# Kernel tuning notes

Hardware: AMD Instinct MI355X
Metric: run time of the kernel (lower is better)

The kernel has to match this reference:

```python
import jax, jax.numpy as jnp
import numpy as np

N_NODES, N_EDGES = 10000, 100000
NODE_DIM, NUM_BASIS = 128, 20
MULS = {0: 128, 1: 64, 2: 32}            # 128x0e + 64x1e + 32x2e
NUM_IRREPS = 224                          # total multiplicity count
HIDDEN = NODE_DIM + NUM_IRREPS            # 352
SPH_DIM = 128 * 1 + 64 * 3 + 32 * 5       # 480
LN_EPS = 1e-5

def _s2_basis():
    # orthonormal (Frobenius) basis of symmetric traceless 3x3 matrices (real l=2)
    s = np.zeros((5, 3, 3)); r2 = 1.0 / np.sqrt(2.0)
    s[0, 0, 1] = s[0, 1, 0] = r2
    s[1, 1, 2] = s[1, 2, 1] = r2
    s[2] = np.diag([-1.0, -1.0, 2.0]) / np.sqrt(6.0)
    s[3, 0, 2] = s[3, 2, 0] = r2
    s[4] = np.diag([1.0, -1.0, 0.0]) * r2
    return s

def _cg_tables():
    # real Clebsch-Gordan tensors for l<=2 built from the invariant tensors
    # delta, Levi-Civita, and the symmetric-traceless basis; unit Frobenius norm (e3nn w3j convention)
    e3 = np.zeros((3, 3, 3))
    e3[0, 1, 2] = e3[1, 2, 0] = e3[2, 0, 1] = 1.0
    e3[0, 2, 1] = e3[2, 1, 0] = e3[1, 0, 2] = -1.0
    S = _s2_basis(); I3 = np.eye(3); I5 = np.eye(5)
    nrm = lambda c: (c / np.linalg.norm(c)).astype(np.float32)
    cg = {(0, 0, 0): np.ones((1, 1, 1), np.float32)}
    cg[(0, 1, 1)] = nrm(I3[None]); cg[(1, 0, 1)] = nrm(I3[:, None, :]); cg[(1, 1, 0)] = nrm(I3[:, :, None])
    cg[(0, 2, 2)] = nrm(I5[None]); cg[(2, 0, 2)] = nrm(I5[:, None, :]); cg[(2, 2, 0)] = nrm(I5[:, :, None])
    cg[(1, 1, 1)] = nrm(e3)
    cg[(1, 1, 2)] = nrm(np.transpose(S, (1, 2, 0)))
    cg[(1, 2, 1)] = nrm(np.transpose(S, (1, 0, 2)))
    cg[(2, 1, 1)] = nrm(S)
    cg[(2, 2, 1)] = nrm(np.einsum('ijk,Mil,Nlj->MNk', e3, S, S))
    cg[(1, 2, 2)] = nrm(np.einsum('iab,Mac,Ncb->iMN', e3, S, S))
    cg[(2, 1, 2)] = nrm(np.einsum('jab,Mac,Ncb->MjN', e3, S, S))
    cg[(2, 2, 2)] = nrm(np.einsum('Mab,Nbc,Pca->MNP', S, S, S))
    return cg

CG = _cg_tables()
PATHS = [(0, 0, 0), (1, 1, 0), (2, 2, 0),
         (0, 1, 1), (1, 0, 1), (1, 1, 1), (1, 2, 1), (2, 1, 1), (2, 2, 1),
         (0, 2, 2), (1, 1, 2), (1, 2, 2), (2, 0, 2), (2, 1, 2), (2, 2, 2)]
FAN = {0: 224, 1: 384, 2: 352}   # e3nn 'element' path-norm fan-in per output irrep
TP_NUMW = sum(MULS[l1] * MULS[l3] for (l1, _, l3) in PATHS)

def _layernorm(x, w, b):
    mu = x.mean(-1, keepdims=True)
    var = ((x - mu) ** 2).mean(-1, keepdims=True)
    return (x - mu) * jax.lax.rsqrt(var + LN_EPS) * w + b

def _o3_layernorm(x, w, b):
    # equivariant layer norm: per-irrep RMS over (mul, m); mean-centering + bias only for scalars
    n = x.shape[0]; outs = []; off = 0; woff = 0
    for l in (0, 1, 2):
        mul, d = MULS[l], 2 * l + 1
        f = x[:, off:off + mul * d].reshape(n, mul, d)
        if l == 0:
            f = f - f.mean(axis=1, keepdims=True)
        nrm = (f * f).mean(axis=(1, 2), keepdims=True)
        f = f * jax.lax.rsqrt(nrm + LN_EPS) * w[woff:woff + mul][None, :, None]
        if l == 0:
            f = f + b[None, :, None]
        outs.append(f.reshape(n, mul * d)); off += mul * d; woff += mul
    return jnp.concatenate(outs, -1)

def _fc_tp(x1, x2, tp_w):
    # FullyConnectedTensorProduct(128x0e+64x1e+32x2e, 1x0e+1x1e+1x2e -> 128x0e+64x1e+32x2e)
    outs = {0: 0.0, 1: 0.0, 2: 0.0}; off = 0
    for (l1, l2, l3) in PATHS:
        m1, m3 = MULS[l1], MULS[l3]
        W = tp_w[off:off + m1 * m3].reshape(m1, m3); off += m1 * m3
        pw = float(np.sqrt((2 * l3 + 1) / FAN[l3]))
        outs[l3] = outs[l3] + pw * jnp.einsum('eum,en,mnk,uw->ewk', x1[l1], x2[l2], jnp.asarray(CG[(l1, l2, l3)]), W, optimize=True)
    e = x2[0].shape[0]
    return jnp.concatenate([outs[l].reshape(e, -1) for l in (0, 1, 2)], -1)

def _forward(x_scalar, x_spherical, rbf, rsh, ln_w, ln_b, o3_w, o3_b,
             mlp_w1, mlp_b1, mlp_w2, mlp_b2, rbf_w, tp_w, edge_index):
    scalar_in = _layernorm(x_scalar, ln_w, ln_b)                # [N,128]
    spherical_in = _o3_layernorm(x_spherical, o3_w, o3_b)       # [N,480]
    h = jax.nn.silu(scalar_in @ mlp_w1 + mlp_b1)
    scalar_out = h @ mlp_w2 + mlp_b2                            # [N,352]
    filt = rbf @ rbf_w                                          # [E,352]
    dst, src = edge_index[0], edge_index[1]
    fo = scalar_out[src] * filt                                 # gather + RBF filter
    gate, msg_scalar = fo[:, :NUM_IRREPS], fo[:, NUM_IRREPS:]
    sph = spherical_in[src]                                     # [E,480]
    e = sph.shape[0]
    # ElementwiseTensorProduct(edge_irreps, 224x0e): per-channel scalar gating
    x1 = {0: (sph[:, :128] * gate[:, :128])[:, :, None],
          1: sph[:, 128:320].reshape(e, 64, 3) * gate[:, 128:192, None],
          2: sph[:, 320:480].reshape(e, 32, 5) * gate[:, 192:224, None]}
    x2 = {0: rsh[:, :1], 1: rsh[:, 1:4], 2: rsh[:, 4:9]}
    msg_sph = _fc_tp(x1, x2, tp_w)                              # [E,480]
    new_scalar = scalar_in.at[dst].add(msg_scalar)
    new_spherical = spherical_in.at[dst].add(msg_sph)
    return new_scalar, new_spherical

def setup_inputs():
    key = jax.random.key(0)
    ks = jax.random.split(key, 9)
    return {
        'x_scalar': jax.random.normal(ks[0], (N_NODES, NODE_DIM), jnp.float32),
        'x_spherical': jax.random.normal(ks[1], (N_NODES, SPH_DIM), jnp.float32),
        'rbf': jax.random.uniform(ks[2], (N_EDGES, NUM_BASIS), jnp.float32),
        'rsh': jax.random.normal(ks[3], (N_EDGES, 9), jnp.float32),
        'edge_index': jax.random.randint(ks[4], (2, N_EDGES), 0, N_NODES, dtype=jnp.int32),
        'ln_w': jnp.ones((NODE_DIM,), jnp.float32),
        'ln_b': jnp.zeros((NODE_DIM,), jnp.float32),
        'o3_w': jnp.ones((NUM_IRREPS,), jnp.float32),
        'o3_b': jnp.zeros((128,), jnp.float32),
        'mlp_w1': jax.random.normal(ks[5], (NODE_DIM, NODE_DIM), jnp.float32) / np.sqrt(NODE_DIM),
        'mlp_b1': jnp.zeros((NODE_DIM,), jnp.float32),
        'mlp_w2': jax.random.normal(ks[6], (NODE_DIM, HIDDEN), jnp.float32) / np.sqrt(NODE_DIM),
        'mlp_b2': jnp.zeros((HIDDEN,), jnp.float32),
        'rbf_w': jax.random.normal(ks[7], (NUM_BASIS, HIDDEN), jnp.float32) / np.sqrt(NUM_BASIS),
        'tp_w': jax.random.normal(ks[8], (TP_NUMW,), jnp.float32),
    }

def reference(x_scalar, x_spherical, rbf, rsh, edge_index, ln_w, ln_b, o3_w, o3_b,
              mlp_w1, mlp_b1, mlp_w2, mlp_b2, rbf_w, tp_w):
    return _forward(x_scalar, x_spherical, rbf, rsh, ln_w, ln_b, o3_w, o3_b,
                    mlp_w1, mlp_b1, mlp_w2, mlp_b2, rbf_w, tp_w, edge_index)
```

## Files before the change

kernel.cpp:

```cpp
#include <hip/hip_runtime.h>

#define NN 10000
#define NE 100000
#define ND 128
#define NB 20
#define NIR 224
#define NH 352
#define SD 480
#define BS 512
#define ET 16
#define NTILES (NE / ET)

#define CR   0.70710678118654752f
#define CA   0.40824829046386302f
#define HA   0.20412414523193151f
#define HR   0.35355339059327376f
#define C110 0.57735026918962576f
#define C220 0.44721359549995794f
#define C111 0.40824829046386302f
#define C11X 0.44721359549995794f
#define C221 0.36514837167011074f
#define C222 0.58554004376912270f
#define S32  0.86602540378443865f
#define PW0  0.066815310478106094f
#define PW1  0.088388347648318447f
#define PW2  0.11918321088232916f

typedef __bf16 v8bf __attribute__((ext_vector_type(8)));
typedef unsigned short us8v __attribute__((ext_vector_type(8)));
typedef float f32x4 __attribute__((ext_vector_type(4)));

__device__ __forceinline__ unsigned short f2bfc(float f) {
  __bf16 h = (__bf16)f;
  return __builtin_bit_cast(unsigned short, h);
}
__device__ __forceinline__ float bf2f(unsigned short h) {
  unsigned int u = ((unsigned int)h) << 16;
  return __builtin_bit_cast(float, u);
}

__device__ __forceinline__ float warpReduceSum(float v) {
  #pragma unroll
  for (int off = 32; off > 0; off >>= 1) v += __shfl_down(v, off, 64);
  return v;
}

__device__ __forceinline__ int t2tT(int t) {
  if (t < 128) return t;
  if (t < 320) { int c = t - 128; return 128 + (c % 3) * 64 + c / 3; }
  int c = t - 320; return 320 + (c % 5) * 32 + c / 5;
}

__global__ __launch_bounds__(256) void sort_hist(const int* __restrict__ ei, int* __restrict__ cnt) {
  int e = blockIdx.x * 256 + threadIdx.x;
  if (e < NE) atomicAdd(&cnt[ei[e]], 1);
}

__global__ __launch_bounds__(1024) void sort_scan(const int* __restrict__ cnt, int* __restrict__ cursor) {
  __shared__ int part[1024];
  const int t = threadIdx.x;
  int loc[10]; int s = 0;
  #pragma unroll
  for (int j = 0; j < 10; ++j) { int idx = t * 10 + j; int v = (idx < NN) ? cnt[idx] : 0; loc[j] = s; s += v; }
  part[t] = s; __syncthreads();
  for (int d = 1; d < 1024; d <<= 1) {
    int v = (t >= d) ? part[t - d] : 0; __syncthreads();
    part[t] += v; __syncthreads();
  }
  int off = part[t] - s;
  #pragma unroll
  for (int j = 0; j < 10; ++j) { int idx = t * 10 + j; if (idx < NN) cursor[idx] = off + loc[j]; }
}

__global__ __launch_bounds__(256) void sort_scatter(
    const int* __restrict__ ei, int* __restrict__ cursor, int* __restrict__ es_eid) {
  int e = blockIdx.x * 256 + threadIdx.x;
  if (e < NE) {
    int d = ei[e];
    int pos = atomicAdd(&cursor[d], 1);
    es_eid[pos] = e;
  }
}

__global__ __launch_bounds__(128) void node_ln_kernel(
    const float* __restrict__ xs, const float* __restrict__ xsph,
    const float* __restrict__ lnw, const float* __restrict__ lnb,
    const float* __restrict__ o3w, const float* __restrict__ o3b,
    float* __restrict__ s_in, float* __restrict__ sphT,
    float* __restrict__ out0)
{
  const int n = blockIdx.x, t = threadIdx.x;
  __shared__ float red[4];

  auto reduce2 = [&](float a, float b) {
    a = warpReduceSum(a); b = warpReduceSum(b);
    if ((t & 63) == 0) { red[(t >> 6) * 2] = a; red[(t >> 6) * 2 + 1] = b; }
    __syncthreads();
    float ra = red[0] + red[2], rb = red[1] + red[3];
    __syncthreads();
    return make_float2(ra, rb);
  };

  float x = xs[n * ND + t];
  float2 sr = reduce2(x, x * x);
  float mu = sr.x * (1.f / ND);
  float var = sr.y * (1.f / ND) - mu * mu;
  float y = (x - mu) * rsqrtf(var + 1e-5f) * lnw[t] + lnb[t];
  s_in[n * ND + t] = y; out0[n * ND + t] = y;

  float f = xsph[n * SD + t];
  float2 r0 = reduce2(f, f * f);
  float m0 = r0.x * (1.f / 128.f);
  float nrm0 = r0.y * (1.f / 128.f) - m0 * m0;
  float y0 = (f - m0) * rsqrtf(nrm0 + 1e-5f) * o3w[t] + o3b[t];
  sphT[n * SD + t] = y0;

  float f1a = xsph[n * SD + 128 + t];
  float f1b = (t < 64) ? xsph[n * SD + 256 + t] : 0.f;
  float2 r1 = reduce2(f1a * f1a + f1b * f1b, 0.f);
  float rs1 = rsqrtf(r1.x * (1.f / 192.f) + 1e-5f);
  sphT[n * SD + t2tT(128 + t)] = f1a * rs1 * o3w[128 + t / 3];
  if (t < 64)
    sphT[n * SD + t2tT(256 + t)] = f1b * rs1 * o3w[128 + (128 + t) / 3];

  float f2a = xsph[n * SD + 320 + t];
  float f2b = (t < 32) ? xsph[n * SD + 448 + t] : 0.f;
  float2 r2 = reduce2(f2a * f2a + f2b * f2b, 0.f);
  float rs2 = rsqrtf(r2.x * (1.f / 160.f) + 1e-5f);
  sphT[n * SD + t2tT(320 + t)] = f2a * rs2 * o3w[192 + t / 5];
  if (t < 32)
    sphT[n * SD + t2tT(448 + t)] = f2b * rs2 * o3w[192 + (128 + t) / 5];
}

#define NPB 8
__global__ __launch_bounds__(256) void mlp_kernel(
    const float* __restrict__ s_in, const float* __restrict__ w1,
    const float* __restrict__ b1, const float* __restrict__ w2,
    const float* __restrict__ b2, float* __restrict__ s_out)
{
  __shared__ float sIn[NPB][ND];
  __shared__ float sH[NPB][ND];
  const int t = threadIdx.x;
  const int n0 = blockIdx.x * NPB;
  for (int i = t; i < NPB * ND; i += 256) sIn[i >> 7][i & 127] = s_in[n0 * ND + i];
  __syncthreads();
  {
    const int j = t & 127, g = t >> 7;
    float acc[4] = {0.f, 0.f, 0.f, 0.f};
    for (int k = 0; k < ND; ++k) {
      float w = w1[k * ND + j];
      #pragma unroll
      for (int i = 0; i < 4; ++i) acc[i] = fmaf(sIn[g + 2 * i][k], w, acc[i]);
    }
    #pragma unroll
    for (int i = 0; i < 4; ++i) {
      float z = acc[i] + b1[j];
      sH[g + 2 * i][j] = z / (1.f + __expf(-z));
    }
  }
  __syncthreads();
  for (int jb = 0; jb < 2; ++jb) {
    int j = jb * 256 + t;
    if (j < NH) {
      float acc[NPB];
      #pragma unroll
      for (int i = 0; i < NPB; ++i) acc[i] = b2[j];
      for (int k = 0; k < ND; ++k) {
        float w = w2[k * NH + j];
        #pragma unroll
        for (int i = 0; i < NPB; ++i) acc[i] = fmaf(sH[i][k], w, acc[i]);
      }
      #pragma unroll
      for (int i = 0; i < NPB; ++i) s_out[(n0 + i) * NH + j] = acc[i];
    }
  }
}

__device__ __forceinline__ float wc0(const float* w, int u, int j) {
  int off = (u < 128) ? u * 128 : (u < 192) ? 16384 + (u - 128) * 128 : 24576 + (u - 192) * 128;
  return w[off + j];
}
__device__ __forceinline__ float wc1(const float* w, int u, int j) {
  int off = (u < 128) ? 28672 + u * 64 : (u < 192) ? 36864 + (u - 128) * 64
          : (u < 256) ? 40960 + (u - 192) * 64 : (u < 320) ? 45056 + (u - 256) * 64
          : (u < 352) ? 49152 + (u - 320) * 64 : 51200 + (u - 352) * 64;
  return w[off + j];
}
__device__ __forceinline__ float wc2(const float* w, int u, int j) {
  int off = (u < 128) ? 53248 + u * 32 : (u < 192) ? 57344 + (u - 128) * 32
          : (u < 256) ? 59392 + (u - 192) * 32 : (u < 288) ? 61440 + (u - 256) * 32
          : (u < 320) ? 62464 + (u - 288) * 32 : 63488 + (u - 320) * 32;
  return w[off + j];
}

__global__ __launch_bounds__(256) void prep_w_kernel(
    const float* __restrict__ tpw, const float* __restrict__ rbf_w,
    unsigned short* __restrict__ W0g, unsigned short* __restrict__ W1g,
    unsigned short* __restrict__ W2g, unsigned short* __restrict__ Wfq)
{
  int gid = blockIdx.x * 256 + threadIdx.x;
  int i = gid & 7, lane = (gid >> 3) & 63;
  int r = lane & 15, kl = lane >> 4;
  if (gid < 28672) {
    int fid = gid >> 9, kk = fid >> 3, wid = fid & 7;
    W0g[gid] = f2bfc(wc0(tpw, kk * 32 + kl * 8 + i, wid * 16 + r));
  } else if (gid < 53248) {
    int g = gid - 28672, fid = g >> 9, kk = fid >> 2, nt = fid & 3;
    W1g[g] = f2bfc(wc1(tpw, kk * 32 + kl * 8 + i, nt * 16 + r));
  } else if (gid < 65536) {
    int g = gid - 53248, fid = g >> 9, q = fid >> 2, kh = (fid >> 1) & 1, ntc = fid & 1;
    int kk = kh * 6 + q;
    W2g[g] = (kk < 11) ? f2bfc(wc2(tpw, kk * 32 + kl * 8 + i, ntc * 16 + r)) : (unsigned short)0;
  } else if (gid < 77824) {
    int g = gid - 65536, fid = g >> 9, q = fid >> 3, wid = fid & 7;
    int t22 = wid + q * 8, k = kl * 8 + i;
    Wfq[g] = (t22 < 22 && k < 20) ? f2bfc(rbf_w[k * NH + t22 * 16 + r]) : (unsigned short)0;
  }
}

template<int M>
__device__ __forceinline__ void emit_dot(unsigned short* dst, const unsigned short* x1,
                                         const int* offs, const float* cf) {
  us8v xv[M];
  #pragma unroll
  for (int m = 0; m < M; ++m) xv[m] = *(const us8v*)&x1[offs[m]];
  v8bf o;
  #pragma unroll
  for (int i = 0; i < 8; ++i) {
    float a = 0.f;
    #pragma unroll
    for (int m = 0; m < M; ++m) a = fmaf(cf[m], bf2f(xv[m][i]), a);
    o[i] = (__bf16)a;
  }
  *(us8v*)dst = __builtin_bit_cast(us8v, o);
}

#define TSW(e, idx) ((idx) ^ (((e) & 7) << 3))

__device__ __forceinline__ void build0_item(unsigned short* Tb, const unsigned short* x1,
                                            const float* R, int e, int ub) {
  int u0 = ub * 8;
  unsigned short* dst = Tb + TSW(e, e * 384 + u0);
  if (u0 < 128) {
    float cf[1] = { PW0 * R[0] };
    int offs[1] = { u0 };
    emit_dot<1>(dst, x1, offs, cf);
  } else if (u0 < 192) {
    int m0 = u0 - 128;
    float cf[3] = { PW0 * C110 * R[1], PW0 * C110 * R[2], PW0 * C110 * R[3] };
    int offs[3] = { 128 + m0, 192 + m0, 256 + m0 };
    emit_dot<3>(dst, x1, offs, cf);
  } else {
    int m0 = u0 - 192;
    float cf[5] = { PW0 * C220 * R[4], PW0 * C220 * R[5], PW0 * C220 * R[6],
                    PW0 * C220 * R[7], PW0 * C220 * R[8] };
    int offs[5] = { 320 + m0, 352 + m0, 384 + m0, 416 + m0, 448 + m0 };
    emit_dot<5>(dst, x1, offs, cf);
  }
}

template<int k>
__device__ __forceinline__ void build1_item(unsigned short* Tb, const unsigned short* x1,
                                            const float* R, int e, int ub) {
  int u0 = ub * 8;
  unsigned short* dst = Tb + TSW(e, e * 384 + u0);
  const float s = R[0], v0 = R[1], v1 = R[2], v2 = R[3];
  const float w0 = R[4], w1 = R[5], w2 = R[6], w3 = R[7], w4 = R[8];
  if (u0 < 128) {
    float cf[1] = { PW1 * C110 * R[1 + k] };
    int offs[1] = { u0 };
    emit_dot<1>(dst, x1, offs, cf);
  } else if (u0 < 192) {
    float cf[1] = { PW1 * C110 * s };
    int offs[1] = { 128 + k * 64 + (u0 - 128) };
    emit_dot<1>(dst, x1, offs, cf);
  } else if (u0 < 256) {
    constexpr int ka = (k + 1) % 3, kb = (k + 2) % 3;
    int m0 = u0 - 192;
    float cf[2] = { PW1 * C111 * R[1 + kb], -PW1 * C111 * R[1 + ka] };
    int offs[2] = { 128 + ka * 64 + m0, 128 + kb * 64 + m0 };
    emit_dot<2>(dst, x1, offs, cf);
  } else if (u0 < 320) {
    int m0 = u0 - 256;
    float cf[3];
    if constexpr (k == 0) { cf[0] = PW1*C11X*(-CA*w2 + CR*w4); cf[1] = PW1*C11X*CR*w0; cf[2] = PW1*C11X*CR*w3; }
    else if constexpr (k == 1) { cf[0] = PW1*C11X*CR*w0; cf[1] = PW1*C11X*(-CA*w2 - CR*w4); cf[2] = PW1*C11X*CR*w1; }
    else { cf[0] = PW1*C11X*CR*w3; cf[1] = PW1*C11X*CR*w1; cf[2] = PW1*C11X*2.f*CA*w2; }
    int offs[3] = { 128 + m0, 192 + m0, 256 + m0 };
    emit_dot<3>(dst, x1, offs, cf);
  } else if (u0 < 352) {
    int m0 = u0 - 320;
    if constexpr (k == 0) {
      float cf[4] = { PW1*C11X*CR*v1, PW1*C11X*(-CA*v0), PW1*C11X*CR*v2, PW1*C11X*CR*v0 };
      int offs[4] = { 320 + m0, 384 + m0, 416 + m0, 448 + m0 };
      emit_dot<4>(dst, x1, offs, cf);
    } else if constexpr (k == 1) {
      float cf[4] = { PW1*C11X*CR*v0, PW1*C11X*CR*v2, PW1*C11X*(-CA*v1), PW1*C11X*(-CR*v1) };
      int offs[4] = { 320 + m0, 352 + m0, 384 + m0, 448 + m0 };
      emit_dot<4>(dst, x1, offs, cf);
    } else {
      float cf[3] = { PW1*C11X*CR*v1, PW1*C11X*2.f*CA*v2, PW1*C11X*CR*v0 };
      int offs[3] = { 352 + m0, 384 + m0, 416 + m0 };
      emit_dot<3>(dst, x1, offs, cf);
    }
  } else {
    int m0 = u0 - 352;
    if constexpr (k == 0) {
      float cf[5] = { PW1*C221*0.5f*w3, PW1*C221*(S32*w2 + 0.5f*w4), PW1*C221*(-S32*w1),
                      PW1*C221*(-0.5f*w0), PW1*C221*(-0.5f*w1) };
      int offs[5] = { 320 + m0, 352 + m0, 384 + m0, 416 + m0, 448 + m0 };
      emit_dot<5>(dst, x1, offs, cf);
    } else if constexpr (k == 1) {
      float cf[5] = { PW1*C221*(-0.5f*w1), PW1*C221*0.5f*w0, PW1*C221*S32*w3,
                      PW1*C221*(-S32*w2 + 0.5f*w4), PW1*C221*(-0.5f*w3) };
      int offs[5] = { 320 + m0, 352 + m0, 384 + m0, 416 + m0, 448 + m0 };
      emit_dot<5>(dst, x1, offs, cf);
    } else {
      float cf[4] = { PW1*C221*(-w4), PW1*C221*(-0.5f*w3), PW1*C221*0.5f*w1, PW1*C221*w0 };
      int offs[4] = { 320 + m0, 352 + m0, 416 + m0, 448 + m0 };
      emit_dot<4>(dst, x1, offs, cf);
    }
  }
}

template<int K>
__device__ __forceinline__ void build2_item(unsigned short* Tb, const unsigned short* x1,
                                            const float* R, int e, int ub) {
  int u0 = ub * 8;
  unsigned short* dst = Tb + TSW(e, e * 384 + u0);
  const float s = R[0], v0 = R[1], v1 = R[2], v2 = R[3];
  const float w0 = R[4], w1 = R[5], w2 = R[6], w3 = R[7], w4 = R[8];
  if (u0 < 128) {
    float cf[1] = { PW2 * C220 * R[4 + K] };
    int offs[1] = { u0 };
    emit_dot<1>(dst, x1, offs, cf);
  } else if (u0 < 192) {
    int m0 = u0 - 128;
    if constexpr (K == 0) {
      float cf[2] = { PW2*C11X*CR*v1, PW2*C11X*CR*v0 };
      int offs[2] = { 128 + m0, 192 + m0 };
      emit_dot<2>(dst, x1, offs, cf);
    } else if constexpr (K == 1) {
      float cf[2] = { PW2*C11X*CR*v2, PW2*C11X*CR*v1 };
      int offs[2] = { 192 + m0, 256 + m0 };
      emit_dot<2>(dst, x1, offs, cf);
    } else if constexpr (K == 2) {
      float cf[3] = { PW2*C11X*(-CA*v0), PW2*C11X*(-CA*v1), PW2*C11X*2.f*CA*v2 };
      int offs[3] = { 128 + m0, 192 + m0, 256 + m0 };
      emit_dot<3>(dst, x1, offs, cf);
    } else if constexpr (K == 3) {
      float cf[2] = { PW2*C11X*CR*v2, PW2*C11X*CR*v0 };
      int offs[2] = { 128 + m0, 256 + m0 };
      emit_dot<2>(dst, x1, offs, cf);
    } else {
      float cf[2] = { PW2*C11X*CR*v0, PW2*C11X*(-CR*v1) };
      int offs[2] = { 128 + m0, 192 + m0 };
      emit_dot<2>(dst, x1, offs, cf);
    }
  } else if (u0 < 256) {
    int m0 = u0 - 192;
    if constexpr (K == 2) {
      float cf[2] = { PW2*C221*S32*w1, PW2*C221*(-S32*w3) };
      int offs[2] = { 128 + m0, 192 + m0 };
      emit_dot<2>(dst, x1, offs, cf);
    } else {
      float cf[3];
      if constexpr (K == 0) { cf[0]=PW2*C221*(-0.5f*w3); cf[1]=PW2*C221*0.5f*w1; cf[2]=PW2*C221*w4; }
      else if constexpr (K == 1) { cf[0]=PW2*C221*(-S32*w2 - 0.5f*w4); cf[1]=PW2*C221*(-0.5f*w0); cf[2]=PW2*C221*0.5f*w3; }
      else if constexpr (K == 3) { cf[0]=PW2*C221*0.5f*w0; cf[1]=PW2*C221*(S32*w2 - 0.5f*w4); cf[2]=PW2*C221*(-0.5f*w1); }
      else { cf[0]=PW2*C221*0.5f*w1; cf[1]=PW2*C221*0.5f*w3; cf[2]=PW2*C221*(-w0); }
      int offs[3] = { 128 + m0, 192 + m0, 256 + m0 };
      emit_dot<3>(dst, x1, offs, cf);
    }
  } else if (u0 < 288) {
    int m0 = u0 - 256;
    float cf[1] = { PW2 * C220 * s };
    int offs[1] = { 320 + K * 32 + m0 };
    emit_dot<1>(dst, x1, offs, cf);
  } else if (u0 < 320) {
    int m0 = u0 - 288;
    if constexpr (K == 0) {
      float cf[3] = { PW2*C221*0.5f*v1, PW2*C221*(-0.5f*v0), PW2*C221*v2 };
      int offs[3] = { 352 + m0, 416 + m0, 448 + m0 };
      emit_dot<3>(dst, x1, offs, cf);
    } else if constexpr (K == 1) {
      float cf[4] = { PW2*C221*(-0.5f*v1), PW2*C221*(-S32*v0), PW2*C221*0.5f*v2, PW2*C221*(-0.5f*v0) };
      int offs[4] = { 320 + m0, 384 + m0, 416 + m0, 448 + m0 };
      emit_dot<4>(dst, x1, offs, cf);
    } else if constexpr (K == 2) {
      float cf[2] = { PW2*C221*S32*v0, PW2*C221*(-S32*v1) };
      int offs[2] = { 352 + m0, 416 + m0 };
      emit_dot<2>(dst, x1, offs, cf);
    } else if constexpr (K == 3) {
      float cf[4] = { PW2*C221*0.5f*v0, PW2*C221*(-0.5f*v2), PW2*C221*S32*v1, PW2*C221*(-0.5f*v1) };
      int offs[4] = { 320 + m0, 352 + m0, 384 + m0, 448 + m0 };
      emit_dot<4>(dst, x1, offs, cf);
    } else {
      float cf[3] = { PW2*C221*(-v2), PW2*C221*0.5f*v0, PW2*C221*0.5f*v1 };
      int offs[3] = { 320 + m0, 352 + m0, 416 + m0 };
      emit_dot<3>(dst, x1, offs, cf);
    }
  } else {
    int m0 = u0 - 320;
    if constexpr (K == 0) {
      float cf[4] = { PW2*C222*(-CA*w2), PW2*C222*HR*w3, PW2*C222*(-CA*w0), PW2*C222*HR*w1 };
      int offs[4] = { 320 + m0, 352 + m0, 384 + m0, 416 + m0 };
      emit_dot<4>(dst, x1, offs, cf);
    } else if constexpr (K == 4) {
      float cf[4] = { PW2*C222*(-HR*w1), PW2*C222*(-CA*w4), PW2*C222*HR*w3, PW2*C222*(-CA*w2) };
      int offs[4] = { 352 + m0, 384 + m0, 416 + m0, 448 + m0 };
      emit_dot<4>(dst, x1, offs, cf);
    } else {
      float cf[5];
      if constexpr (K == 1) { cf[0]=PW2*C222*HR*w3; cf[1]=PW2*C222*(HA*w2 - HR*w4); cf[2]=PW2*C222*HA*w1; cf[3]=PW2*C222*HR*w0; cf[4]=PW2*C222*(-HR*w1); }
      else if constexpr (K == 2) { cf[0]=PW2*C222*(-CA*w0); cf[1]=PW2*C222*HA*w1; cf[2]=PW2*C222*CA*w2; cf[3]=PW2*C222*HA*w3; cf[4]=PW2*C222*(-CA*w4); }
      else { cf[0]=PW2*C222*HR*w1; cf[1]=PW2*C222*HR*w0; cf[2]=PW2*C222*HA*w3; cf[3]=PW2*C222*(HA*w2 + HR*w4); cf[4]=PW2*C222*HR*w3; }
      int offs[5] = { 320 + m0, 352 + m0, 384 + m0, 416 + m0, 448 + m0 };
      emit_dot<5>(dst, x1, offs, cf);
    }
  }
}

__global__ __launch_bounds__(BS, 8) void tp_fused_kernel(
    const float* __restrict__ rbf, const float* __restrict__ rsh,
    const int* __restrict__ ei, const float* __restrict__ s_out,
    const float* __restrict__ sphT,
    const unsigned short* __restrict__ W0g, const unsigned short* __restrict__ W1g,
    const unsigned short* __restrict__ W2g, const unsigned short* __restrict__ Wfq,
    float* __restrict__ out0, unsigned short* __restrict__ msgT)
{
  __shared__ __align__(16) unsigned char smem[40640];
  unsigned short* Tb0 = (unsigned short*)smem;
  unsigned short* Tb1 = (unsigned short*)(smem + 12288);
  unsigned short* gateU = (unsigned short*)smem;
  unsigned short* rbfpadU = (unsigned short*)(smem + 12288);
  unsigned short* X1u = (unsigned short*)(smem + 24576);
  float* RshF = (float*)(smem + 39936);
  int* EdstS = (int*)(smem + 40512);
  int* EsrcS = (int*)(smem + 40576);

  const int tid = threadIdx.x;
  const int wid = tid >> 6, lane = tid & 63;
  const int r = lane & 15, kl = lane >> 4;
  const int be = tid >> 5, th = tid & 31;

  auto MFMA = [](v8bf a, v8bf b, f32x4 c) {
    return __builtin_amdgcn_mfma_f32_16x16x32_bf16(a, b, c, 0, 0, 0);
  };
  auto ldw = [&](const unsigned short* base, int fid) {
    return __builtin_bit_cast(v8bf, *(const us8v*)&base[fid * 512 + lane * 8]);
  };

  auto mfma_l0 = [&](const unsigned short* T, long ebase) {
    f32x4 acc = {0.f, 0.f, 0.f, 0.f};
    #pragma unroll
    for (int kk = 0; kk < 7; ++kk) {
      v8bf b = ldw(W0g, kk * 8 + wid);
      us8v a = *(const us8v*)&T[TSW(r, r * 384 + kl * 8 + kk * 32)];
      acc = MFMA(__builtin_bit_cast(v8bf, a), b, acc);
    }
    int col = wid * 16 + r;
    #pragma unroll
    for (int j = 0; j < 4; ++j)
      msgT[(ebase + kl * 4 + j) * SD + col] = f2bfc(acc[j]);
  };

  auto mfma_l1 = [&](const unsigned short* T, int k, long ebase) {
    if (wid < 4) {
      const int nt = wid;
      f32x4 acc = {0.f, 0.f, 0.f, 0.f};
      #pragma unroll
      for (int kk = 0; kk < 12; ++kk) {
        v8bf b = ldw(W1g, kk * 4 + nt);
        us8v a = *(const us8v*)&T[TSW(r, r * 384 + kl * 8 + kk * 32)];
        acc = MFMA(__builtin_bit_cast(v8bf, a), b, acc);
      }
      int col = 128 + k * 64 + nt * 16 + r;
      #pragma unroll
      for (int j = 0; j < 4; ++j)
        msgT[(ebase + kl * 4 + j) * SD + col] = f2bfc(acc[j]);
    }
  };

  auto mfma_l2 = [&](const unsigned short* T, int K, long ebase) {
    if (wid < 2) {
      const int ntc = wid;
      f32x4 acc = {0.f, 0.f, 0.f, 0.f};
      #pragma unroll
      for (int kk = 0; kk < 11; ++kk) {
        v8bf b = ldw(W2g, (kk % 6) * 4 + (kk / 6) * 2 + ntc);
        us8v a = *(const us8v*)&T[TSW(r, r * 384 + kk * 32 + kl * 8)];
        acc = MFMA(__builtin_bit_cast(v8bf, a), b, acc);
      }
      int col = 320 + K * 32 + ntc * 16 + r;
      #pragma unroll
      for (int j = 0; j < 4; ++j)
        msgT[(ebase + kl * 4 + j) * SD + col] = f2bfc(acc[j]);
    }
  };

  for (int tile = blockIdx.x; tile < NTILES; tile += gridDim.x) {
    const int e0 = tile * ET;
    const long ebase = e0;
    for (int i = tid; i < ET; i += BS) { EdstS[i] = ei[e0 + i]; EsrcS[i] = ei[NE + e0 + i]; }
    for (int i = tid; i < ET * 9; i += BS) RshF[i] = rsh[(long)e0 * 9 + i];
    for (int i = tid; i < ET * 32; i += BS) {
      int e = i >> 5, b = i & 31;
      rbfpadU[e * 40 + b] = (b < 20) ? f2bfc(rbf[(long)(e0 + e) * NB + b]) : (unsigned short)0;
    }
    __syncthreads();
    {
      us8v ra = *(const us8v*)&rbfpadU[r * 40 + kl * 8];
      v8bf av = __builtin_bit_cast(v8bf, ra);
      #pragma unroll
      for (int q = 0; q < 3; ++q) {
        int t22 = wid + q * 8;
        if (t22 < 22) {
          v8bf b = ldw(Wfq, q * 8 + wid);
          f32x4 acc = {0.f, 0.f, 0.f, 0.f};
          acc = MFMA(av, b, acc);
          int gi = t22 * 16 + r;
          #pragma unroll
          for (int j = 0; j < 4; ++j) {
            int e = kl * 4 + j;
            float so = s_out[(long)EsrcS[e] * NH + gi];
            float val = acc[j] * so;
            if (t22 < 14) gateU[e * 232 + gi] = f2bfc(val);
            else unsafeAtomicAdd(&out0[(long)EdstS[e] * ND + (gi - 224)], val);
          }
        }
      }
    }
    __syncthreads();
    float Rr[9];
    #pragma unroll
    for (int j = 0; j < 9; ++j) Rr[j] = RshF[be * 9 + j];
    const unsigned short* x1p = &X1u[be * 480];
    {
      long srow = (long)EsrcS[be] * SD;
      #pragma unroll
      for (int rep = 0; rep < 2; ++rep) {
        int cb = th + rep * 32;
        if (rep == 0 || th < 28) {
          int c0 = cb * 8;
          int gidx = (c0 < 128) ? c0 : (c0 < 320) ? 128 + (c0 & 63) : 192 + (c0 & 31);
          us8v gv = *(const us8v*)&gateU[be * 232 + gidx];
          const float4 sa = *(const float4*)&sphT[srow + c0];
          const float4 sb = *(const float4*)&sphT[srow + c0 + 4];
          float sv[8] = {sa.x, sa.y, sa.z, sa.w, sb.x, sb.y, sb.z, sb.w};
          v8bf o;
          #pragma unroll
          for (int i = 0; i < 8; ++i) o[i] = (__bf16)(sv[i] * bf2f(gv[i]));
          *(us8v*)&X1u[be * 480 + c0] = __builtin_bit_cast(us8v, o);
        }
      }
    }
    __syncthreads();
    if (th < 28) build0_item(Tb0, x1p, Rr, be, th);
    __syncthreads();
    build1_item<0>(Tb1, x1p, Rr, be, th);
    if (th < 16) build1_item<0>(Tb1, x1p, Rr, be, th + 32);
    mfma_l0(Tb0, ebase); __syncthreads();
    build1_item<1>(Tb0, x1p, Rr, be, th);
    if (th < 16) build1_item<1>(Tb0, x1p, Rr, be, th + 32);
    mfma_l1(Tb1, 0, ebase); __syncthreads();
    build1_item<2>(Tb1, x1p, Rr, be, th);
    if (th < 16) build1_item<2>(Tb1, x1p, Rr, be, th + 32);
    mfma_l1(Tb0, 1, ebase); __syncthreads();
    build2_item<0>(Tb0, x1p, Rr, be, th);
    if (th < 12) build2_item<0>(Tb0, x1p, Rr, be, th + 32);
    mfma_l1(Tb1, 2, ebase); __syncthreads();
    build2_item<1>(Tb1, x1p, Rr, be, th);
    if (th < 12) build2_item<1>(Tb1, x1p, Rr, be, th + 32);
    mfma_l2(Tb0, 0, ebase); __syncthreads();
    build2_item<2>(Tb0, x1p, Rr, be, th);
    if (th < 12) build2_item<2>(Tb0, x1p, Rr, be, th + 32);
    mfma_l2(Tb1, 1, ebase); __syncthreads();
    build2_item<3>(Tb1, x1p, Rr, be, th);
    if (th < 12) build2_item<3>(Tb1, x1p, Rr, be, th + 32);
    mfma_l2(Tb0, 2, ebase); __syncthreads();
    build2_item<4>(Tb0, x1p, Rr, be, th);
    if (th < 12) build2_item<4>(Tb0, x1p, Rr, be, th + 32);
    mfma_l2(Tb1, 3, ebase); __syncthreads();
    mfma_l2(Tb0, 4, ebase); __syncthreads();
  }
}

__global__ __launch_bounds__(512) void gather_kernel(
    const float* __restrict__ sphT, const unsigned short* __restrict__ msgT,
    const int* __restrict__ cnt, const int* __restrict__ cursor,
    const int* __restrict__ es_eid, float* __restrict__ out1)
{
  __shared__ float sumT[SD];
  __shared__ int eids[160];
  __shared__ int s_deg;
  const int n = blockIdx.x, t = threadIdx.x;
  if (t == 0) {
    int d = cnt[n];
    s_deg = (d > 160) ? 160 : d;
  }
  __syncthreads();
  int deg = s_deg;
  int start = cursor[n] - cnt[n];
  for (int i = t; i < deg; i += 512) eids[i] = es_eid[start + i];
  __syncthreads();
  if (t < SD) {
    float acc = 0.f;
    for (int i = 0; i < deg; ++i)
      acc += bf2f(msgT[(long)eids[i] * SD + t]);
    sumT[t] = acc;
  }
  __syncthreads();
  if (t < SD) {
    int tT = t2tT(t);
    out1[(long)n * SD + t] = sphT[(long)n * SD + tT] + sumT[tT];
  }
}

extern "C" void kernel_launch(void* const* d_in, const int* in_sizes, int n_in,
                              void* d_out, int out_size, void* d_ws, size_t ws_size,
                              hipStream_t stream)
{
  const float* xs   = (const float*)d_in[0];
  const float* xsph = (const float*)d_in[1];
  const float* rbf  = (const float*)d_in[2];
  const float* rsh  = (const float*)d_in[3];
  const int*   ei   = (const int*)d_in[4];
  const float* lnw  = (const float*)d_in[5];
  const float* lnb  = (const float*)d_in[6];
  const float* o3w  = (const float*)d_in[7];
  const float* o3b  = (const float*)d_in[8];
  const float* w1   = (const float*)d_in[9];
  const float* b1   = (const float*)d_in[10];
  const float* w2   = (const float*)d_in[11];
  const float* b2   = (const float*)d_in[12];
  const float* rbfw = (const float*)d_in[13];
  const float* tpw  = (const float*)d_in[14];

  float* out0 = (float*)d_out;
  float* out1 = out0 + (size_t)NN * ND;

  float* ws      = (float*)d_ws;
  float* s_in    = ws;
  float* sphT    = ws + (size_t)NN * ND;
  float* s_out   = ws + (size_t)NN * (ND + SD);
  unsigned short* msgT = (unsigned short*)(ws + (size_t)NN * (ND + SD + NH));
  unsigned short* wbase = msgT + (size_t)NE * SD;
  unsigned short* W0g = wbase;
  unsigned short* W1g = wbase + 28672;
  unsigned short* W2g = wbase + 53248;
  unsigned short* Wfq = wbase + 65536;
  int* ibase  = (int*)(wbase + 77824);
  int* cnt    = ibase;
  int* cursor = ibase + 10000;
  int* es_eid = ibase + 20000;

  hipMemsetAsync(cnt, 0, (size_t)NN * sizeof(int), stream);
  sort_hist<<<(NE + 255) / 256, 256, 0, stream>>>(ei, cnt);
  sort_scan<<<1, 1024, 0, stream>>>(cnt, cursor);
  sort_scatter<<<(NE + 255) / 256, 256, 0, stream>>>(ei, cursor, es_eid);
  prep_w_kernel<<<304, 256, 0, stream>>>(tpw, rbfw, W0g, W1g, W2g, Wfq);
  node_ln_kernel<<<NN, 128, 0, stream>>>(xs, xsph, lnw, lnb, o3w, o3b, s_in, sphT, out0);
  mlp_kernel<<<NN / NPB, 256, 0, stream>>>(s_in, w1, b1, w2, b2, s_out);
  tp_fused_kernel<<<1024, BS, 0, stream>>>(rbf, rsh, ei, s_out, sphT,
                                           W0g, W1g, W2g, Wfq, out0, msgT);
  gather_kernel<<<NN, 512, 0, stream>>>(sphT, msgT, cnt, cursor, es_eid, out1);
}
```

Measured before the change: 664.0 us.

## Quad-buffer TP stages so all waves run MFMA in parallel; pack gather loads

Shared memory grows from two to four staging tiles, which lets several build stages and several MFMA stages run in the same barrier interval. The idle waves (wid>=4 or >=2) now take work on other tiles, so the barrier count per tile falls from ten to six. The added LDS lowers occupancy, so launch bounds go from 8 to 4 and the grid from 1024 to 512 blocks. Separately, the gather kernel reads two bf16 values per 32-bit load, using 240 threads instead of 480.

```diff
diff --git a/kernel.cpp b/kernel.cpp
--- a/kernel.cpp
+++ b/kernel.cpp
@@ -421,7 +421,7 @@
   }
 }
 
-__global__ __launch_bounds__(BS, 8) void tp_fused_kernel(
+__global__ __launch_bounds__(BS, 4) void tp_fused_kernel(
     const float* __restrict__ rbf, const float* __restrict__ rsh,
     const int* __restrict__ ei, const float* __restrict__ s_out,
     const float* __restrict__ sphT,
@@ -429,15 +429,17 @@
     const unsigned short* __restrict__ W2g, const unsigned short* __restrict__ Wfq,
     float* __restrict__ out0, unsigned short* __restrict__ msgT)
 {
-  __shared__ __align__(16) unsigned char smem[40640];
-  unsigned short* Tb0 = (unsigned short*)smem;
-  unsigned short* Tb1 = (unsigned short*)(smem + 12288);
+  __shared__ __align__(16) unsigned char smem[65216];
+  unsigned short* S0 = (unsigned short*)smem;
+  unsigned short* S1 = (unsigned short*)(smem + 12288);
+  unsigned short* S2 = (unsigned short*)(smem + 24576);
+  unsigned short* S3 = (unsigned short*)(smem + 36864);
   unsigned short* gateU = (unsigned short*)smem;
   unsigned short* rbfpadU = (unsigned short*)(smem + 12288);
-  unsigned short* X1u = (unsigned short*)(smem + 24576);
-  float* RshF = (float*)(smem + 39936);
-  int* EdstS = (int*)(smem + 40512);
-  int* EsrcS = (int*)(smem + 40576);
+  unsigned short* X1u = (unsigned short*)(smem + 49152);
+  float* RshF = (float*)(smem + 64512);
+  int* EdstS = (int*)(smem + 65088);
+  int* EsrcS = (int*)(smem + 65152);
 
   const int tid = threadIdx.x;
   const int wid = tid >> 6, lane = tid & 63;
@@ -465,38 +467,32 @@
       msgT[(ebase + kl * 4 + j) * SD + col] = f2bfc(acc[j]);
   };
 
-  auto mfma_l1 = [&](const unsigned short* T, int k, long ebase) {
-    if (wid < 4) {
-      const int nt = wid;
-      f32x4 acc = {0.f, 0.f, 0.f, 0.f};
-      #pragma unroll
-      for (int kk = 0; kk < 12; ++kk) {
-        v8bf b = ldw(W1g, kk * 4 + nt);
-        us8v a = *(const us8v*)&T[TSW(r, r * 384 + kl * 8 + kk * 32)];
-        acc = MFMA(__builtin_bit_cast(v8bf, a), b, acc);
-      }
-      int col = 128 + k * 64 + nt * 16 + r;
-      #pragma unroll
-      for (int j = 0; j < 4; ++j)
-        msgT[(ebase + kl * 4 + j) * SD + col] = f2bfc(acc[j]);
-    }
+  auto mfma_l1w = [&](const unsigned short* T, int k, int nt, long ebase) {
+    f32x4 acc = {0.f, 0.f, 0.f, 0.f};
+    #pragma unroll
+    for (int kk = 0; kk < 12; ++kk) {
+      v8bf b = ldw(W1g, kk * 4 + nt);
+      us8v a = *(const us8v*)&T[TSW(r, r * 384 + kl * 8 + kk * 32)];
+      acc = MFMA(__builtin_bit_cast(v8bf, a), b, acc);
+    }
+    int col = 128 + k * 64 + nt * 16 + r;
+    #pragma unroll
+    for (int j = 0; j < 4; ++j)
+      msgT[(ebase + kl * 4 + j) * SD + col] = f2bfc(acc[j]);
   };
 
-  auto mfma_l2 = [&](const unsigned short* T, int K, long ebase) {
-    if (wid < 2) {
-      const int ntc = wid;
-      f32x4 acc = {0.f, 0.f, 0.f, 0.f};
-      #pragma unroll
-      for (int kk = 0; kk < 11; ++kk) {
-        v8bf b = ldw(W2g, (kk % 6) * 4 + (kk / 6) * 2 + ntc);
-        us8v a = *(const us8v*)&T[TSW(r, r * 384 + kk * 32 + kl * 8)];
-        acc = MFMA(__builtin_bit_cast(v8bf, a), b, acc);
-      }
-      int col = 320 + K * 32 + ntc * 16 + r;
-      #pragma unroll
-      for (int j = 0; j < 4; ++j)
-        msgT[(ebase + kl * 4 + j) * SD + col] = f2bfc(acc[j]);
-    }
+  auto mfma_l2w = [&](const unsigned short* T, int K, int ntc, long ebase) {
+    f32x4 acc = {0.f, 0.f, 0.f, 0.f};
+    #pragma unroll
+    for (int kk = 0; kk < 11; ++kk) {
+      v8bf b = ldw(W2g, (kk % 6) * 4 + (kk / 6) * 2 + ntc);
+      us8v a = *(const us8v*)&T[TSW(r, r * 384 + kk * 32 + kl * 8)];
+      acc = MFMA(__builtin_bit_cast(v8bf, a), b, acc);
+    }
+    int col = 320 + K * 32 + ntc * 16 + r;
+    #pragma unroll
+    for (int j = 0; j < 4; ++j)
+      msgT[(ebase + kl * 4 + j) * SD + col] = f2bfc(acc[j]);
   };
 
   for (int tile = blockIdx.x; tile < NTILES; tile += gridDim.x) {
@@ -556,33 +552,38 @@
       }
     }
     __syncthreads();
-    if (th < 28) build0_item(Tb0, x1p, Rr, be, th);
-    __syncthreads();
-    build1_item<0>(Tb1, x1p, Rr, be, th);
-    if (th < 16) build1_item<0>(Tb1, x1p, Rr, be, th + 32);
-    mfma_l0(Tb0, ebase); __syncthreads();
-    build1_item<1>(Tb0, x1p, Rr, be, th);
-    if (th < 16) build1_item<1>(Tb0, x1p, Rr, be, th + 32);
-    mfma_l1(Tb1, 0, ebase); __syncthreads();
-    build1_item<2>(Tb1, x1p, Rr, be, th);
-    if (th < 16) build1_item<2>(Tb1, x1p, Rr, be, th + 32);
-    mfma_l1(Tb0, 1, ebase); __syncthreads();
-    build2_item<0>(Tb0, x1p, Rr, be, th);
-    if (th < 12) build2_item<0>(Tb0, x1p, Rr, be, th + 32);
-    mfma_l1(Tb1, 2, ebase); __syncthreads();
-    build2_item<1>(Tb1, x1p, Rr, be, th);
-    if (th < 12) build2_item<1>(Tb1, x1p, Rr, be, th + 32);
-    mfma_l2(Tb0, 0, ebase); __syncthreads();
-    build2_item<2>(Tb0, x1p, Rr, be, th);
-    if (th < 12) build2_item<2>(Tb0, x1p, Rr, be, th + 32);
-    mfma_l2(Tb1, 1, ebase); __syncthreads();
-    build2_item<3>(Tb1, x1p, Rr, be, th);
-    if (th < 12) build2_item<3>(Tb1, x1p, Rr, be, th + 32);
-    mfma_l2(Tb0, 2, ebase); __syncthreads();
-    build2_item<4>(Tb0, x1p, Rr, be, th);
-    if (th < 12) build2_item<4>(Tb0, x1p, Rr, be, th + 32);
-    mfma_l2(Tb1, 3, ebase); __syncthreads();
-    mfma_l2(Tb0, 4, ebase); __syncthreads();
+    if (th < 28) build0_item(S0, x1p, Rr, be, th);
+    __syncthreads();
+    build1_item<0>(S1, x1p, Rr, be, th);
+    if (th < 16) build1_item<0>(S1, x1p, Rr, be, th + 32);
+    else         build1_item<1>(S2, x1p, Rr, be, th - 16);
+    build1_item<1>(S2, x1p, Rr, be, th + 16);
+    mfma_l0(S0, ebase);
+    __syncthreads();
+    build1_item<2>(S3, x1p, Rr, be, th);
+    if (th < 16) build1_item<2>(S3, x1p, Rr, be, th + 32);
+    else         build2_item<0>(S0, x1p, Rr, be, th - 16);
+    if (th < 28) build2_item<0>(S0, x1p, Rr, be, th + 16);
+    if (wid < 4) mfma_l1w(S1, 0, wid, ebase);
+    else         mfma_l1w(S2, 1, wid - 4, ebase);
+    __syncthreads();
+    build2_item<1>(S1, x1p, Rr, be, th);
+    if (th < 12) build2_item<1>(S1, x1p, Rr, be, th + 32);
+    else         build2_item<2>(S2, x1p, Rr, be, th - 12);
+    if (th < 24) build2_item<2>(S2, x1p, Rr, be, th + 20);
+    if (wid < 4)      mfma_l1w(S3, 2, wid, ebase);
+    else if (wid < 6) mfma_l2w(S0, 0, wid - 4, ebase);
+    __syncthreads();
+    build2_item<3>(S3, x1p, Rr, be, th);
+    if (th < 12) build2_item<3>(S3, x1p, Rr, be, th + 32);
+    else         build2_item<4>(S0, x1p, Rr, be, th - 12);
+    if (th < 24) build2_item<4>(S0, x1p, Rr, be, th + 20);
+    if (wid < 2)      mfma_l2w(S1, 1, wid, ebase);
+    else if (wid < 4) mfma_l2w(S2, 2, wid - 2, ebase);
+    __syncthreads();
+    if (wid < 2)      mfma_l2w(S3, 3, wid, ebase);
+    else if (wid < 4) mfma_l2w(S0, 4, wid - 2, ebase);
+    __syncthreads();
   }
 }
 
@@ -604,11 +605,14 @@
   int start = cursor[n] - cnt[n];
   for (int i = t; i < deg; i += 512) eids[i] = es_eid[start + i];
   __syncthreads();
-  if (t < SD) {
-    float acc = 0.f;
-    for (int i = 0; i < deg; ++i)
-      acc += bf2f(msgT[(long)eids[i] * SD + t]);
-    sumT[t] = acc;
+  if (t < 240) {
+    float a0 = 0.f, a1 = 0.f;
+    for (int i = 0; i < deg; ++i) {
+      unsigned v = *(const unsigned*)&msgT[(long)eids[i] * SD + 2 * t];
+      a0 += bf2f((unsigned short)(v & 0xffffu));
+      a1 += bf2f((unsigned short)(v >> 16));
+    }
+    sumT[2 * t] = a0; sumT[2 * t + 1] = a1;
   }
   __syncthreads();
   if (t < SD) {
@@ -662,7 +666,7 @@
   prep_w_kernel<<<304, 256, 0, stream>>>(tpw, rbfw, W0g, W1g, W2g, Wfq);
   node_ln_kernel<<<NN, 128, 0, stream>>>(xs, xsph, lnw, lnb, o3w, o3b, s_in, sphT, out0);
   mlp_kernel<<<NN / NPB, 256, 0, stream>>>(s_in, w1, b1, w2, b2, s_out);
-  tp_fused_kernel<<<1024, BS, 0, stream>>>(rbf, rsh, ei, s_out, sphT,
-                                           W0g, W1g, W2g, Wfq, out0, msgT);
+  tp_fused_kernel<<<512, BS, 0, stream>>>(rbf, rsh, ei, s_out, sphT,
+                                          W0g, W1g, W2g, Wfq, out0, msgT);
   gather_kernel<<<NN, 512, 0, stream>>>(sphT, msgT, cnt, cursor, es_eid, out1);
 }
```

Result: no change. 660.6 us (-0.5%).
